# Kernel optimization log

Measured on AMD Instinct MI355X. Metric: run time of the kernel, lower is better.

## Reference

```python
import jax, jax.numpy as jnp
import numpy as np

B, S, T = 32, 32, 64          # docs, sentences/doc, tokens/sentence
E, HW, HS = 128, 128, 128     # embed, word hidden, sentence hidden
CW, CS = 128, 128             # attention context sizes
V, NC = 50000, 8              # vocab, classes


def setup_inputs() -> dict:
    key = jax.random.key(0)
    ks = iter(jax.random.split(key, 40))
    x = jax.random.randint(next(ks), (B, S, T), 1, V, dtype=jnp.int32)
    wl = jax.random.randint(next(ks), (B, S), 8, T + 1)   # word lengths
    sl = jax.random.randint(next(ks), (B,), 8, S + 1)     # sentence counts
    tmask = jnp.arange(T)[None, None, :] < wl[:, :, None]
    smask = (jnp.arange(S)[None, :] < sl[:, None])[:, :, None]
    x = jnp.where(tmask & smask, x, 0)                     # 0 = pad token

    def u(shape, scale=0.1):
        return jax.random.uniform(next(ks), shape, jnp.float32, -scale, scale)

    d = {"x": x, "emb": u((V, E))}
    # GRU params in torch layout: W_ih [3H,D] (r|z|n), W_hh [3H,H], biases [3H]
    for pre, Din, H in [("wf", E, HW), ("wb", E, HW), ("sf", 2 * HW, HS), ("sb", 2 * HW, HS)]:
        d[pre + "_Wih"] = u((3 * H, Din))
        d[pre + "_Whh"] = u((3 * H, H))
        d[pre + "_bih"] = u((3 * H,))
        d[pre + "_bhh"] = u((3 * H,))
    d["wproj_W"] = u((CW, 2 * HW)); d["wproj_b"] = u((CW,)); d["wctx"] = u((CW,))
    d["sproj_W"] = u((CS, 2 * HS)); d["sproj_b"] = u((CS,)); d["sctx"] = u((CS,))
    d["fc_W"] = u((NC, 2 * HS)); d["fc_b"] = u((NC,))
    return d


def seq_lens_2d(tok):
    # torch get_sequence_lens: T - trailing zeros, 1 if all zero
    nz = tok != 0
    any_nz = jnp.any(nz, axis=1)
    last = tok.shape[1] - jnp.argmax(nz[:, ::-1], axis=1)
    return jnp.where(any_nz, last, 1)


def doc_lens(x):
    # torch get_num_sentences_lens: S - trailing all-zero sentences
    nz = jnp.any(x != 0, axis=2)  # [B,S]
    any_nz = jnp.any(nz, axis=1)
    last = x.shape[1] - jnp.argmax(nz[:, ::-1], axis=1)
    return jnp.where(any_nz, last, 1)


def run_gru(x, lens, Wih, Whh, bih, bhh, reverse):
    # x: [N,Tm,D]; emulates pack_padded: state frozen / output zeroed beyond len
    N, Tm, _ = x.shape
    H = Whh.shape[1]
    xp = jnp.einsum('ntd,gd->ntg', x, Wih) + bih  # [N,Tm,3H]

    def step(h, inp):
        xg, t = inp
        hg = h @ Whh.T + bhh
        xr, xz, xn = jnp.split(xg, 3, axis=-1)
        hr, hz, hn = jnp.split(hg, 3, axis=-1)
        r = jax.nn.sigmoid(xr + hr)
        z = jax.nn.sigmoid(xz + hz)
        n = jnp.tanh(xn + r * hn)
        h_new = (1 - z) * n + z * h
        valid = (t < lens)[:, None]
        h_new = jnp.where(valid, h_new, h)
        return h_new, jnp.where(valid, h_new, 0.0)

    h0 = jnp.zeros((N, H), x.dtype)
    _, ys = jax.lax.scan(step, h0, (jnp.swapaxes(xp, 0, 1), jnp.arange(Tm)), reverse=reverse)
    return jnp.swapaxes(ys, 0, 1)  # [N,Tm,H]


def bigru(x, lens, pf, pb):
    return jnp.concatenate([run_gru(x, lens, *pf, reverse=False),
                            run_gru(x, lens, *pb, reverse=True)], axis=-1)


def attn_pool(out, lens, Wp, bp, ctx):
    # faithful to torch: softmax over padded positions up to max(lens)
    # (pad_packed pads to max length; padded outputs are zero but score=tanh(b)@c)
    Tm = out.shape[1]
    scores = jnp.tanh(out @ Wp.T + bp) @ ctx            # [N,Tm]
    valid = jnp.arange(Tm)[None, :] < jnp.max(lens)
    attn = jax.nn.softmax(jnp.where(valid, scores, -jnp.inf), axis=-1)
    return jnp.einsum('nt,nth->nh', attn, out)


def han_forward(x, emb,
                wf_Wih, wf_Whh, wf_bih, wf_bhh, wb_Wih, wb_Whh, wb_bih, wb_bhh,
                wproj_W, wproj_b, wctx,
                sf_Wih, sf_Whh, sf_bih, sf_bhh, sb_Wih, sb_Whh, sb_bih, sb_bhh,
                sproj_W, sproj_b, sctx, fc_W, fc_b):
    Bx, Sx, Tx = x.shape
    xw = x.reshape(-1, Tx)                      # [B*S, T]
    wlens = seq_lens_2d(xw)
    slens = doc_lens(x)
    we = emb[xw]                                # [B*S, T, E]
    wout = bigru(we, wlens, (wf_Wih, wf_Whh, wf_bih, wf_bhh),
                 (wb_Wih, wb_Whh, wb_bih, wb_bhh))     # [B*S, T, 2HW]
    sent = attn_pool(wout, wlens, wproj_W, wproj_b, wctx)  # [B*S, 2HW]
    sent = sent.reshape(Bx, Sx, -1)
    sout = bigru(sent, slens, (sf_Wih, sf_Whh, sf_bih, sf_bhh),
                 (sb_Wih, sb_Whh, sb_bih, sb_bhh))     # [B, S, 2HS]
    doc = attn_pool(sout, slens, sproj_W, sproj_b, sctx)   # [B, 2HS]
    return doc @ fc_W.T + fc_b                             # [B, NC]


def reference(x, emb,
              wf_Wih, wf_Whh, wf_bih, wf_bhh, wb_Wih, wb_Whh, wb_bih, wb_bhh,
              wproj_W, wproj_b, wctx,
              sf_Wih, sf_Whh, sf_bih, sf_bhh, sb_Wih, sb_Whh, sb_bih, sb_bhh,
              sproj_W, sproj_b, sctx, fc_W, fc_b):
    return han_forward(x, emb,
                       wf_Wih, wf_Whh, wf_bih, wf_bhh, wb_Wih, wb_Whh, wb_bih, wb_bhh,
                       wproj_W, wproj_b, wctx,
                       sf_Wih, sf_Whh, sf_bih, sf_bhh, sb_Wih, sb_Whh, sb_bih, sb_bhh,
                       sproj_W, sproj_b, sctx, fc_W, fc_b)
```

## Files before the change

### kernel.cpp

```cpp
#include <hip/hip_runtime.h>
#include <hip/hip_bf16.h>

typedef unsigned short ushort_t;
typedef __attribute__((ext_vector_type(4))) float floatx4;
typedef __attribute__((ext_vector_type(8))) short short8;

#define L2E 1.4426950408889634f

__device__ __forceinline__ float bf2f(ushort_t u) {
    union { unsigned int i; float f; } v; v.i = ((unsigned int)u) << 16; return v.f;
}
__device__ __forceinline__ ushort_t f2bf(float f) {
    union { float f; unsigned int i; } v; v.f = f;
    unsigned int i = v.i;
    i += 0x7fffu + ((i >> 16) & 1u);
    return (ushort_t)(i >> 16);
}
__device__ __forceinline__ float fexp2(float x) {
#if __has_builtin(__builtin_amdgcn_exp2f)
    return __builtin_amdgcn_exp2f(x);
#else
    return __expf(x * 0.6931471805599453f);
#endif
}
__device__ __forceinline__ float frcp(float x) {
#if __has_builtin(__builtin_amdgcn_rcpf)
    return __builtin_amdgcn_rcpf(x);
#else
    return 1.f / x;
#endif
}
__device__ __forceinline__ float sig2(float a)  { return frcp(1.f + fexp2(a)); }
__device__ __forceinline__ float tanh2(float y) { return 1.f - 2.f * frcp(1.f + fexp2(y)); }

__device__ __forceinline__ unsigned int packbf(float a, float b) {
    float2 t; t.x = a; t.y = b;
    __hip_bfloat162 h = __float22bfloat162_rn(t);
    union { __hip_bfloat162 h; unsigned int u; } v; v.h = h; return v.u;
}

__device__ __forceinline__ floatx4 MFMA16(short8 a, short8 b, floatx4 c) {
    return __builtin_amdgcn_mfma_f32_16x16x32_bf16(a, b, c, 0, 0, 0);
}

__device__ __forceinline__ void bar_lds() {
    __builtin_amdgcn_s_waitcnt(0xc07f);
    __builtin_amdgcn_s_barrier();
}

#define XIDX(c, m) ((((c) * 16) + ((m) ^ ((c) & 15))) * 8)

__global__ __launch_bounds__(64) void lens_kernel(const int* __restrict__ x,
                                                  const unsigned int* __restrict__ raw,
                                                  int* wlens, int* slens, int* dmax,
                                                  int* flag) {
    int b = blockIdx.x, s = threadIdx.x;
    if (b == 32) {
        int c = 0;
        for (int i = 0; i < 16; ++i) {
            unsigned int v = raw[s * 16 + i];
            unsigned int e = (v >> 7) & 0xFFu;
            if (e > 0x7Bu) ++c;
        }
        c += __shfl_xor(c, 1);  c += __shfl_xor(c, 2);  c += __shfl_xor(c, 4);
        c += __shfl_xor(c, 8);  c += __shfl_xor(c, 16); c += __shfl_xor(c, 32);
        if (s == 0) *flag = (c > 64) ? 1 : 0;
        return;
    }
    int last = 0;
    if (s < 32) {
        const int* tok = x + (b * 32 + s) * 64;
        for (int t = 0; t < 64; t += 4) {
            int4 v = *(const int4*)(tok + t);
            if (v.x) last = t + 1;
            if (v.y) last = t + 2;
            if (v.z) last = t + 3;
            if (v.w) last = t + 4;
        }
        wlens[b * 32 + s] = last ? last : 1;
    }
    int len = (s < 32) ? (last ? last : 1) : 0;
    int lm = len;
    for (int off = 32; off; off >>= 1) lm = max(lm, __shfl_xor(lm, off));
    unsigned long long mask = __ballot(s < 32 && last > 0);
    if (s == 0) {
        slens[b] = mask ? (63 - (int)__clzll(mask) + 1) : 1;
        dmax[b] = lm;
    }
}

struct ConvArgs {
    const void* src[25];
    int dstoff[25];
    int count[25];
    int cumblk[26];
    int mode[25];
    int rowdiv[25];
};

__global__ __launch_bounds__(256) void convert_kernel(ConvArgs a, ushort_t* __restrict__ dst,
                                                      const int* __restrict__ flag) {
    int b = blockIdx.x;
    int lo = 0, hi = 24;
    while (lo < hi) { int mid = (lo + hi + 1) >> 1; if (a.cumblk[mid] <= b) lo = mid; else hi = mid - 1; }
    int j = lo;
    int base = (b - a.cumblk[j]) * 2048 + threadIdx.x * 8;
    if (base >= a.count[j]) return;
    ushort_t* out = dst + a.dstoff[j] + base;
    int m = a.mode[j], rd = a.rowdiv[j];
    float f[8];
    if (*flag) {
        const float* s = (const float*)a.src[j] + base;
        float4 v0 = *(const float4*)s;
        float4 v1 = *(const float4*)(s + 4);
        f[0] = v0.x; f[1] = v0.y; f[2] = v0.z; f[3] = v0.w;
        f[4] = v1.x; f[5] = v1.y; f[6] = v1.z; f[7] = v1.w;
    } else {
        const ushort_t* s = (const ushort_t*)a.src[j] + base;
        uint4 v = *(const uint4*)s;
        const ushort_t* u = (const ushort_t*)&v;
        #pragma unroll
        for (int e = 0; e < 8; ++e) f[e] = bf2f(u[e]);
    }
    union { ushort_t u[8]; uint4 v; } o;
    #pragma unroll
    for (int e = 0; e < 8; ++e) {
        float sc = 1.f;
        if (m == 2) sc = 2.f * L2E;
        else if (m == 1) sc = ((base + e) / rd < 256) ? -L2E : 2.f * L2E;
        o.u[e] = f2bf(f[e] * sc);
    }
    *(uint4*)out = o.v;
}

__global__ __launch_bounds__(512, 2) void word_gru_kernel(
        const int* __restrict__ x, const ushort_t* __restrict__ emb,
        const ushort_t* __restrict__ Wih_f, const ushort_t* __restrict__ Whh_f,
        const ushort_t* __restrict__ bih_f, const ushort_t* __restrict__ bhh_f,
        const ushort_t* __restrict__ Wih_b, const ushort_t* __restrict__ Whh_b,
        const ushort_t* __restrict__ bih_b, const ushort_t* __restrict__ bhh_b,
        const int* __restrict__ lens, ushort_t* __restrict__ out) {
    const int T = 64;
    __shared__ ushort_t h_buf[2][2048];
    __shared__ float bsum_lds[256];
    __shared__ float bihn_lds[128];
    __shared__ float bhhn_lds[128];
    __shared__ int tok_lds[1024];

    int tid = threadIdx.x;
    int d = blockIdx.y;
    int n0 = blockIdx.x * 16;
    const ushort_t* Wih = d ? Wih_b : Wih_f;
    const ushort_t* Whh = d ? Whh_b : Whh_f;
    const ushort_t* bih = d ? bih_b : bih_f;
    const ushort_t* bhh = d ? bhh_b : bhh_f;
    int lane = tid & 63, wave = tid >> 6;
    int l15 = lane & 15, l4 = (lane >> 4) & 3;
    int jt = wave * 16;
    int j0 = jt + l4 * 4;

    for (int i = tid; i < 1024; i += 512) {
        int t = i >> 4, s = i & 15;
        tok_lds[i] = x[(n0 + s) * 64 + t];
    }
    if (tid < 256) bsum_lds[tid] = bf2f(bih[tid]) + bf2f(bhh[tid]);
    else if (tid < 384) {
        bihn_lds[tid - 256] = bf2f(bih[tid]);
        bhhn_lds[tid - 256] = bf2f(bhh[tid]);
    }
    { uint2 z = {0u, 0u}; *(uint2*)&h_buf[0][tid * 4] = z; }

    short8 wr[4], wz[4], wn[4], ur[4], uz[4], un[4];
    #pragma unroll
    for (int kf = 0; kf < 4; ++kf) {
        int col = kf * 32 + l4 * 8;
        wr[kf] = *(const short8*)(Wih + (size_t)(jt + l15) * 128 + col);
        wz[kf] = *(const short8*)(Wih + (size_t)(128 + jt + l15) * 128 + col);
        wn[kf] = *(const short8*)(Wih + (size_t)(256 + jt + l15) * 128 + col);
        ur[kf] = *(const short8*)(Whh + (size_t)(jt + l15) * 128 + col);
        uz[kf] = *(const short8*)(Whh + (size_t)(128 + jt + l15) * 128 + col);
        un[kf] = *(const short8*)(Whh + (size_t)(256 + jt + l15) * 128 + col);
    }
    __syncthreads();

    floatx4 br  = *(floatx4*)&bsum_lds[j0];
    floatx4 bz  = *(floatx4*)&bsum_lds[128 + j0];
    floatx4 bxn = *(floatx4*)&bihn_lds[j0];
    floatx4 bhn = *(floatx4*)&bhhn_lds[j0];
    int lv = lens[n0 + l15];
    float hreg[4] = {0.f, 0.f, 0.f, 0.f};

    short8 xc[4], xn_[4];
    {
        int t0 = d ? (T - 1) : 0;
        size_t rb = (size_t)tok_lds[t0 * 16 + l15] * 128 + l4 * 8;
        #pragma unroll
        for (int kf = 0; kf < 4; ++kf)
            xc[kf] = *(const short8*)(emb + rb + kf * 32);
    }

    for (int ti = 0; ti < T; ++ti) {
        int t = d ? (T - 1 - ti) : ti;
        bool have_next = (ti + 1) < T;
        if (have_next) {
            int tn = d ? (T - 2 - ti) : (ti + 1);
            size_t rb = (size_t)tok_lds[tn * 16 + l15] * 128 + l4 * 8;
            #pragma unroll
            for (int kf = 0; kf < 4; ++kf)
                xn_[kf] = *(const short8*)(emb + rb + kf * 32);
        }
        short8 hb[4];
        #pragma unroll
        for (int kf = 0; kf < 4; ++kf)
            hb[kf] = *(const short8*)&h_buf[ti & 1][XIDX(kf * 4 + l4, l15)];
        floatx4 arx = br, azx = bz, axn = bxn;
        floatx4 arh = {0.f, 0.f, 0.f, 0.f}, azh = {0.f, 0.f, 0.f, 0.f}, ahn = bhn;
        #pragma unroll
        for (int kf = 0; kf < 4; ++kf) {
            arx = MFMA16(wr[kf], xc[kf], arx);
            azx = MFMA16(wz[kf], xc[kf], azx);
            axn = MFMA16(wn[kf], xc[kf], axn);
        }
        #pragma unroll
        for (int kf = 0; kf < 4; ++kf) {
            arh = MFMA16(ur[kf], hb[kf], arh);
            azh = MFMA16(uz[kf], hb[kf], azh);
            ahn = MFMA16(un[kf], hb[kf], ahn);
        }
        bool valid = t < lv;
        float hnew[4];
        #pragma unroll
        for (int i = 0; i < 4; ++i) {
            float r  = sig2(arx[i] + arh[i]);
            float z  = sig2(azx[i] + azh[i]);
            float nn = tanh2(axn[i] + r * ahn[i]);
            hnew[i] = valid ? (nn + z * (hreg[i] - nn)) : hreg[i];
            hreg[i] = hnew[i];
        }
        uint2 h2, o2;
        h2.x = packbf(hnew[0], hnew[1]);
        h2.y = packbf(hnew[2], hnew[3]);
        o2.x = valid ? h2.x : 0u;
        o2.y = valid ? h2.y : 0u;
        *(uint2*)&h_buf[(ti & 1) ^ 1][XIDX(j0 >> 3, l15) + (j0 & 7)] = h2;
        *(uint2*)(out + ((size_t)(n0 + l15) * T + t) * 256 + d * 128 + j0) = o2;
        if (have_next) {
            #pragma unroll
            for (int kf = 0; kf < 4; ++kf) xc[kf] = xn_[kf];
        }
        bar_lds();
    }
}

__global__ __launch_bounds__(256) void spt_gemm_kernel(const ushort_t* __restrict__ A,
                                                       const ushort_t* __restrict__ Bf_,
                                                       const ushort_t* __restrict__ biasf,
                                                       ushort_t* __restrict__ Tf_,
                                                       const ushort_t* __restrict__ Bb_,
                                                       const ushort_t* __restrict__ biasb,
                                                       ushort_t* __restrict__ Tb_) {
    __shared__ ushort_t As[64 * 256];
    __shared__ ushort_t Bs[64 * 256];
    const int K = 256;
    int tid = threadIdx.x;
    int by = blockIdx.y;
    bool sb = by >= 6;
    int n0 = (sb ? by - 6 : by) * 64;
    const ushort_t* B = sb ? Bb_ : Bf_;
    const ushort_t* bias = sb ? biasb : biasf;
    ushort_t* Tp = sb ? Tb_ : Tf_;
    int m0 = blockIdx.x * 64;
    for (int idx = tid; idx < 2048; idx += 256) {
        int m = idx & 63, c = idx >> 6;
        *(uint4*)&As[(c * 64 + m) * 8] = *(const uint4*)(A + (size_t)(m0 + m) * K + c * 8);
    }
    for (int idx = tid; idx < 2048; idx += 256) {
        int n = idx & 63, c = idx >> 6;
        *(uint4*)&Bs[(c * 64 + n) * 8] = *(const uint4*)(B + (size_t)(n0 + n) * K + c * 8);
    }
    __syncthreads();
    int lane = tid & 63, wave = tid >> 6;
    int wm = (wave & 1) * 32, wn = (wave >> 1) * 32;
    int l15 = lane & 15, l4 = lane >> 4;
    floatx4 acc[2][2] = {};
    for (int kf = 0; kf < 8; ++kf) {
        int c = kf * 4 + l4;
        short8 a0 = *(const short8*)&As[(c * 64 + wm + l15) * 8];
        short8 a1 = *(const short8*)&As[(c * 64 + wm + 16 + l15) * 8];
        short8 b0 = *(const short8*)&Bs[(c * 64 + wn + l15) * 8];
        short8 b1 = *(const short8*)&Bs[(c * 64 + wn + 16 + l15) * 8];
        acc[0][0] = MFMA16(a0, b0, acc[0][0]);
        acc[0][1] = MFMA16(a0, b1, acc[0][1]);
        acc[1][0] = MFMA16(a1, b0, acc[1][0]);
        acc[1][1] = MFMA16(a1, b1, acc[1][1]);
    }
    for (int nt = 0; nt < 2; ++nt) {
        int n = n0 + wn + nt * 16 + l15;
        float bv = bf2f(bias[n]);
        int jc = n >> 2, ji = n & 3;
        for (int mt = 0; mt < 2; ++mt) {
            int mbase = m0 + wm + mt * 16 + l4 * 4;
            #pragma unroll
            for (int i = 0; i < 4; ++i) {
                int m = mbase + i;
                int doc = m >> 5, t = m & 31;
                size_t dst = ((size_t)((doc >> 4) * 32 + t) * 96 + jc) * 64
                           + (doc & 15) * 4 + ji;
                Tp[dst] = f2bf(acc[mt][nt][i] + bv);
            }
        }
    }
}

__global__ __launch_bounds__(512, 1) void sent_gru_kernel(
        const ushort_t* __restrict__ spT_f, const ushort_t* __restrict__ spT_b,
        const ushort_t* __restrict__ Whh_f, const ushort_t* __restrict__ Whh_b,
        const ushort_t* __restrict__ bhh_f, const ushort_t* __restrict__ bhh_b,
        const int* __restrict__ lens, ushort_t* __restrict__ out) {
    const int T = 32;
    __shared__ ushort_t h_buf[2][2048];
    __shared__ float bhh_lds[384];

    int tid = threadIdx.x;
    int d = blockIdx.y;
    int n0 = blockIdx.x * 16;
    const ushort_t* spT = d ? spT_b : spT_f;
    const ushort_t* Whh = d ? Whh_b : Whh_f;
    const ushort_t* bhh = d ? bhh_b : bhh_f;
    int lane = tid & 63, wave = tid >> 6;
    int l15 = lane & 15, l4 = (lane >> 4) & 3;
    int jt = wave * 16;
    int j0 = jt + l4 * 4;
    int jc = j0 >> 2;

    if (tid < 384) bhh_lds[tid] = bf2f(bhh[tid]);
    { uint2 z = {0u, 0u}; *(uint2*)&h_buf[0][tid * 4] = z; }

    short8 ur[4], uz[4], un[4];
    #pragma unroll
    for (int kf = 0; kf < 4; ++kf) {
        int col = kf * 32 + l4 * 8;
        ur[kf] = *(const short8*)(Whh + (size_t)(jt + l15) * 128 + col);
        uz[kf] = *(const short8*)(Whh + (size_t)(128 + jt + l15) * 128 + col);
        un[kf] = *(const short8*)(Whh + (size_t)(256 + jt + l15) * 128 + col);
    }
    __syncthreads();

    floatx4 br  = *(floatx4*)&bhh_lds[j0];
    floatx4 bz  = *(floatx4*)&bhh_lds[128 + j0];
    floatx4 bhn = *(floatx4*)&bhh_lds[256 + j0];
    int lv = lens[n0 + l15];
    float hreg[4] = {0.f, 0.f, 0.f, 0.f};

    const ushort_t* sp = spT + (size_t)(blockIdx.x * 32) * 96 * 64 + l15 * 4;
    ushort4 xr_c, xz_c, xn_c, xr_n, xz_n, xn_n;
    {
        int t0 = d ? (T - 1) : 0;
        size_t rb = (size_t)t0 * 96 * 64;
        xr_c = *(const ushort4*)(sp + rb + (size_t)jc * 64);
        xz_c = *(const ushort4*)(sp + rb + (size_t)(32 + jc) * 64);
        xn_c = *(const ushort4*)(sp + rb + (size_t)(64 + jc) * 64);
    }

    for (int ti = 0; ti < T; ++ti) {
        int t = d ? (T - 1 - ti) : ti;
        int cur = ti & 1;
        bool have_next = (ti + 1) < T;
        if (have_next) {
            int tn = d ? (T - 2 - ti) : (ti + 1);
            size_t rb = (size_t)tn * 96 * 64;
            xr_n = *(const ushort4*)(sp + rb + (size_t)jc * 64);
            xz_n = *(const ushort4*)(sp + rb + (size_t)(32 + jc) * 64);
            xn_n = *(const ushort4*)(sp + rb + (size_t)(64 + jc) * 64);
        }
        floatx4 ar = br, az = bz, ahn = bhn;
        #pragma unroll
        for (int kf = 0; kf < 4; ++kf) {
            short8 hb = *(const short8*)&h_buf[cur][XIDX(kf * 4 + l4, l15)];
            ar  = MFMA16(ur[kf], hb, ar);
            az  = MFMA16(uz[kf], hb, az);
            ahn = MFMA16(un[kf], hb, ahn);
        }
        float xr[4] = {bf2f(xr_c.x), bf2f(xr_c.y), bf2f(xr_c.z), bf2f(xr_c.w)};
        float xz[4] = {bf2f(xz_c.x), bf2f(xz_c.y), bf2f(xz_c.z), bf2f(xz_c.w)};
        float xn[4] = {bf2f(xn_c.x), bf2f(xn_c.y), bf2f(xn_c.z), bf2f(xn_c.w)};
        bool valid = t < lv;
        float hnew[4];
        #pragma unroll
        for (int i = 0; i < 4; ++i) {
            float r  = sig2(xr[i] + ar[i]);
            float z  = sig2(xz[i] + az[i]);
            float nn = tanh2(xn[i] + r * ahn[i]);
            hnew[i] = valid ? (nn + z * (hreg[i] - nn)) : hreg[i];
            hreg[i] = hnew[i];
        }
        uint2 h2, o2;
        h2.x = packbf(hnew[0], hnew[1]);
        h2.y = packbf(hnew[2], hnew[3]);
        o2.x = valid ? h2.x : 0u;
        o2.y = valid ? h2.y : 0u;
        *(uint2*)&h_buf[cur ^ 1][XIDX(j0 >> 3, l15) + (j0 & 7)] = h2;
        *(uint2*)(out + ((size_t)(n0 + l15) * T + t) * 256 + d * 128 + j0) = o2;
        if (have_next) { xr_c = xr_n; xz_c = xz_n; xn_c = xn_n; }
        bar_lds();
    }
}

#define SP 264
__global__ __launch_bounds__(256) void word_attn_kernel(const ushort_t* __restrict__ wout,
                                                        const ushort_t* __restrict__ W,
                                                        const ushort_t* __restrict__ bias,
                                                        const ushort_t* __restrict__ ctx,
                                                        const int* __restrict__ dmax,
                                                        ushort_t* __restrict__ sent) {
    __shared__ ushort_t tile[64 * SP];
    __shared__ float bc[256];
    __shared__ float sc_lds[64];
    __shared__ float p_lds[64];
    int tid = threadIdx.x, g = blockIdx.x;
    for (int idx = tid; idx < 2048; idx += 256) {
        int row = idx >> 5, k0 = (idx & 31) * 8;
        *(uint4*)&tile[row * SP + k0] = *(const uint4*)(wout + ((size_t)g * 64 + row) * 256 + k0);
    }
    if (tid < 128) bc[tid] = bf2f(bias[tid]);
    else bc[tid] = bf2f(ctx[tid - 128]);
    __syncthreads();
    int lane = tid & 63, wave = tid >> 6;
    int l15 = lane & 15, l4 = (lane >> 4) & 3;
    short8 a[8];
    #pragma unroll
    for (int kf = 0; kf < 8; ++kf)
        a[kf] = *(const short8*)&tile[(wave * 16 + l15) * SP + kf * 32 + l4 * 8];
    floatx4 acc[8];
    #pragma unroll
    for (int nt = 0; nt < 8; ++nt) {
        floatx4 c = {0.f, 0.f, 0.f, 0.f};
        #pragma unroll
        for (int kf = 0; kf < 8; ++kf) {
            short8 b = *(const short8*)(W + (size_t)(nt * 16 + l15) * 256 + kf * 32 + l4 * 8);
            c = MFMA16(a[kf], b, c);
        }
        acc[nt] = c;
    }
    float s[4] = {0.f, 0.f, 0.f, 0.f};
    #pragma unroll
    for (int nt = 0; nt < 8; ++nt) {
        float bv = bc[nt * 16 + l15], cv = bc[128 + nt * 16 + l15];
        #pragma unroll
        for (int i = 0; i < 4; ++i)
            s[i] += tanh2(acc[nt][i] + bv) * cv;
    }
    #pragma unroll
    for (int i = 0; i < 4; ++i) {
        s[i] += __shfl_xor(s[i], 1);
        s[i] += __shfl_xor(s[i], 2);
        s[i] += __shfl_xor(s[i], 4);
        s[i] += __shfl_xor(s[i], 8);
    }
    if (l15 == 0) {
        #pragma unroll
        for (int i = 0; i < 4; ++i) sc_lds[wave * 16 + l4 * 4 + i] = s[i];
    }
    __syncthreads();
    if (tid < 64) {
        int ml = dmax[tid & 31];
        for (int off = 32; off; off >>= 1) ml = max(ml, __shfl_xor(ml, off));
        bool v = tid < ml;
        float sc = v ? sc_lds[tid] : -1e30f;
        float mx = sc;
        for (int off = 32; off; off >>= 1) mx = fmaxf(mx, __shfl_xor(mx, off));
        float e = v ? __expf(sc - mx) : 0.f;
        float sum = e;
        for (int off = 32; off; off >>= 1) sum += __shfl_xor(sum, off);
        p_lds[tid] = e * frcp(fmaxf(sum, 1e-30f));
    }
    __syncthreads();
    float acc2 = 0.f;
    for (int t = 0; t < 64; ++t) acc2 += p_lds[t] * bf2f(tile[t * SP + tid]);
    sent[(size_t)g * 256 + tid] = f2bf(acc2);
}

__global__ __launch_bounds__(256) void sent_attn_fc_kernel(const ushort_t* __restrict__ sout,
                                                           const ushort_t* __restrict__ W,
                                                           const ushort_t* __restrict__ bias,
                                                           const ushort_t* __restrict__ ctx,
                                                           const ushort_t* __restrict__ fcW,
                                                           const ushort_t* __restrict__ fcb,
                                                           const int* __restrict__ slens,
                                                           const int* __restrict__ flagp,
                                                           void* __restrict__ outp) {
    __shared__ ushort_t tile[32 * SP];
    __shared__ float bc[256];
    __shared__ float sc_lds[32];
    __shared__ float p_lds[32];
    __shared__ float dv[256];
    int tid = threadIdx.x, g = blockIdx.x;
    for (int idx = tid; idx < 1024; idx += 256) {
        int row = idx >> 5, k0 = (idx & 31) * 8;
        *(uint4*)&tile[row * SP + k0] = *(const uint4*)(sout + ((size_t)g * 32 + row) * 256 + k0);
    }
    if (tid < 128) bc[tid] = bf2f(bias[tid]);
    else bc[tid] = bf2f(ctx[tid - 128]);
    __syncthreads();
    int lane = tid & 63, wave = tid >> 6;
    int l15 = lane & 15, l4 = (lane >> 4) & 3;
    if (wave < 2) {
        short8 a[8];
        #pragma unroll
        for (int kf = 0; kf < 8; ++kf)
            a[kf] = *(const short8*)&tile[(wave * 16 + l15) * SP + kf * 32 + l4 * 8];
        floatx4 acc[8];
        #pragma unroll
        for (int nt = 0; nt < 8; ++nt) {
            floatx4 c = {0.f, 0.f, 0.f, 0.f};
            #pragma unroll
            for (int kf = 0; kf < 8; ++kf) {
                short8 b = *(const short8*)(W + (size_t)(nt * 16 + l15) * 256 + kf * 32 + l4 * 8);
                c = MFMA16(a[kf], b, c);
            }
            acc[nt] = c;
        }
        float s[4] = {0.f, 0.f, 0.f, 0.f};
        #pragma unroll
        for (int nt = 0; nt < 8; ++nt) {
            float bv = bc[nt * 16 + l15], cv = bc[128 + nt * 16 + l15];
            #pragma unroll
            for (int i = 0; i < 4; ++i)
                s[i] += tanh2(acc[nt][i] + bv) * cv;
        }
        #pragma unroll
        for (int i = 0; i < 4; ++i) {
            s[i] += __shfl_xor(s[i], 1);
            s[i] += __shfl_xor(s[i], 2);
            s[i] += __shfl_xor(s[i], 4);
            s[i] += __shfl_xor(s[i], 8);
        }
        if (l15 == 0) {
            #pragma unroll
            for (int i = 0; i < 4; ++i) sc_lds[wave * 16 + l4 * 4 + i] = s[i];
        }
    }
    __syncthreads();
    if (tid < 32) {
        int ml = slens[tid];
        for (int off = 16; off; off >>= 1) ml = max(ml, __shfl_xor(ml, off, 32));
        bool v = tid < ml;
        float sc = v ? sc_lds[tid] : -1e30f;
        float mx = sc;
        for (int off = 16; off; off >>= 1) mx = fmaxf(mx, __shfl_xor(mx, off, 32));
        float e = v ? __expf(sc - mx) : 0.f;
        float sum = e;
        for (int off = 16; off; off >>= 1) sum += __shfl_xor(sum, off, 32);
        p_lds[tid] = e * frcp(fmaxf(sum, 1e-30f));
    }
    __syncthreads();
    float acc2 = 0.f;
    for (int t = 0; t < 32; ++t) acc2 += p_lds[t] * bf2f(tile[t * SP + tid]);
    dv[tid] = acc2;
    __syncthreads();
    int c = tid >> 5, q0 = (tid & 31) * 8;
    float partial = 0.f;
    #pragma unroll
    for (int q = 0; q < 8; ++q)
        partial += dv[q0 + q] * bf2f(fcW[(size_t)c * 256 + q0 + q]);
    for (int off = 16; off; off >>= 1) partial += __shfl_xor(partial, off, 32);
    if ((tid & 31) == 0) {
        float v = partial + bf2f(fcb[c]);
        if (*flagp) ((float*)outp)[g * 8 + c] = v;
        else        ((ushort_t*)outp)[g * 8 + c] = f2bf(v);
    }
}

extern "C" void kernel_launch(void* const* d_in, const int* in_sizes, int n_in,
                              void* d_out, int out_size, void* d_ws, size_t ws_size,
                              hipStream_t stream) {
    const int* x = (const int*)d_in[0];
    char* ws = (char*)d_ws;

    const size_t O_CONV = 0;
    const size_t O_WOUT = 14680064;
    const size_t O_SENT = 48234496;
    const size_t O_SOUT = 48758784;
    const size_t O_SPTF = 49283072;
    const size_t O_SPTB = 50855936;
    const size_t O_LENS = 52428800;
    const size_t O_SLEN = 52432896;
    const size_t O_DMAX = 52433024;
    const size_t O_FLAG = 52433152;

    ushort_t* conv = (ushort_t*)(ws + O_CONV);
    ushort_t* wout = (ushort_t*)(ws + O_WOUT);
    ushort_t* sent = (ushort_t*)(ws + O_SENT);
    ushort_t* sout = (ushort_t*)(ws + O_SOUT);
    ushort_t* sptf = (ushort_t*)(ws + O_SPTF);
    ushort_t* sptb = (ushort_t*)(ws + O_SPTB);
    int* wlens = (int*)(ws + O_LENS);
    int* slens = (int*)(ws + O_SLEN);
    int* dmax  = (int*)(ws + O_DMAX);
    int* flag  = (int*)(ws + O_FLAG);

    static const int kMode[25]   = {0, 1,1,1,1, 1,1,1,1, 1,1,1,1, 1,1,1,1, 2,2,0, 2,2,0, 0,0};
    static const int kRowdiv[25] = {1, 128,128,1,1, 128,128,1,1, 256,128,1,1, 256,128,1,1,
                                    1,1,1, 1,1,1, 1,1};

    ConvArgs ca;
    ushort_t* cw[25];
    int off = 0, blk = 0;
    for (int i = 1; i <= 25; ++i) {
        int j = i - 1;
        int cnt = in_sizes[i];
        ca.src[j] = d_in[i];
        ca.dstoff[j] = off;
        ca.count[j] = cnt;
        ca.cumblk[j] = blk;
        ca.mode[j] = kMode[j];
        ca.rowdiv[j] = kRowdiv[j];
        cw[j] = conv + off;
        off += cnt;
        blk += (cnt + 2047) / 2048;
    }
    ca.cumblk[25] = blk;

    lens_kernel<<<33, 64, 0, stream>>>(x, (const unsigned int*)d_in[1],
                                       wlens, slens, dmax, flag);
    convert_kernel<<<blk, 256, 0, stream>>>(ca, conv, flag);
    word_gru_kernel<<<dim3(64, 2), 512, 0, stream>>>(
        x, cw[0],
        cw[1], cw[2], cw[3], cw[4],
        cw[5], cw[6], cw[7], cw[8],
        wlens, wout);
    word_attn_kernel<<<1024, 256, 0, stream>>>(wout, cw[17], cw[18], cw[19], dmax, sent);
    spt_gemm_kernel<<<dim3(16, 12), 256, 0, stream>>>(sent, cw[9], cw[11], sptf,
                                                      cw[13], cw[15], sptb);
    sent_gru_kernel<<<dim3(2, 2), 512, 0, stream>>>(
        sptf, sptb, cw[10], cw[14], cw[12], cw[16], slens, sout);
    sent_attn_fc_kernel<<<32, 256, 0, stream>>>(sout, cw[20], cw[21], cw[22],
                                                cw[23], cw[24], slens, flag, d_out);
    (void)n_in; (void)out_size; (void)ws_size;
}
```

Before: 285.7 us.

## Halve sequences per GRU block to double block count for latency-bound recurrences

Both the word-level and sentence-level GRU kernels now process 8 sequences per block instead of 16, so twice as many blocks run (256 instead of 128 for words, 8 instead of 4 for sentences). The MFMA N dimension stays 16, with lanes 8-15 duplicating rows 0-7, and only the first half writes results. A new swizzle macro matches the smaller hidden-state buffer. The aim is to spread the serial recurrence over more compute units on the 256-CU part, at the cost of half-wasted MFMA work and twice the weight loading per sequence.

```diff
diff --git a/kernel.cpp b/kernel.cpp
--- a/kernel.cpp
+++ b/kernel.cpp
@@ -49,6 +49,7 @@
 }
 
 #define XIDX(c, m) ((((c) * 16) + ((m) ^ ((c) & 15))) * 8)
+#define X8(c, m) ((((c) * 8) + ((m) ^ ((c) & 7))) * 8)
 
 __global__ __launch_bounds__(64) void lens_kernel(const int* __restrict__ x,
                                                   const unsigned int* __restrict__ raw,
@@ -141,34 +142,36 @@
         const ushort_t* __restrict__ bih_b, const ushort_t* __restrict__ bhh_b,
         const int* __restrict__ lens, ushort_t* __restrict__ out) {
     const int T = 64;
-    __shared__ ushort_t h_buf[2][2048];
+    __shared__ ushort_t h_buf[2][1024];
     __shared__ float bsum_lds[256];
     __shared__ float bihn_lds[128];
     __shared__ float bhhn_lds[128];
-    __shared__ int tok_lds[1024];
+    __shared__ int tok_lds[512];
 
     int tid = threadIdx.x;
     int d = blockIdx.y;
-    int n0 = blockIdx.x * 16;
+    int n0 = blockIdx.x * 8;
     const ushort_t* Wih = d ? Wih_b : Wih_f;
     const ushort_t* Whh = d ? Whh_b : Whh_f;
     const ushort_t* bih = d ? bih_b : bih_f;
     const ushort_t* bhh = d ? bhh_b : bhh_f;
     int lane = tid & 63, wave = tid >> 6;
     int l15 = lane & 15, l4 = (lane >> 4) & 3;
+    int s8 = l15 & 7;
+    bool sv = l15 < 8;
     int jt = wave * 16;
     int j0 = jt + l4 * 4;
 
-    for (int i = tid; i < 1024; i += 512) {
-        int t = i >> 4, s = i & 15;
-        tok_lds[i] = x[(n0 + s) * 64 + t];
+    {
+        int t = tid >> 3, s = tid & 7;
+        tok_lds[tid] = x[(n0 + s) * 64 + t];
     }
     if (tid < 256) bsum_lds[tid] = bf2f(bih[tid]) + bf2f(bhh[tid]);
     else if (tid < 384) {
         bihn_lds[tid - 256] = bf2f(bih[tid]);
         bhhn_lds[tid - 256] = bf2f(bhh[tid]);
     }
-    { uint2 z = {0u, 0u}; *(uint2*)&h_buf[0][tid * 4] = z; }
+    if (tid < 256) { uint2 z = {0u, 0u}; *(uint2*)&h_buf[0][tid * 4] = z; }
 
     short8 wr[4], wz[4], wn[4], ur[4], uz[4], un[4];
     #pragma unroll
@@ -187,13 +190,13 @@
     floatx4 bz  = *(floatx4*)&bsum_lds[128 + j0];
     floatx4 bxn = *(floatx4*)&bihn_lds[j0];
     floatx4 bhn = *(floatx4*)&bhhn_lds[j0];
-    int lv = lens[n0 + l15];
+    int lv = lens[n0 + s8];
     float hreg[4] = {0.f, 0.f, 0.f, 0.f};
 
     short8 xc[4], xn_[4];
     {
         int t0 = d ? (T - 1) : 0;
-        size_t rb = (size_t)tok_lds[t0 * 16 + l15] * 128 + l4 * 8;
+        size_t rb = (size_t)tok_lds[t0 * 8 + s8] * 128 + l4 * 8;
         #pragma unroll
         for (int kf = 0; kf < 4; ++kf)
             xc[kf] = *(const short8*)(emb + rb + kf * 32);
@@ -204,7 +207,7 @@
         bool have_next = (ti + 1) < T;
         if (have_next) {
             int tn = d ? (T - 2 - ti) : (ti + 1);
-            size_t rb = (size_t)tok_lds[tn * 16 + l15] * 128 + l4 * 8;
+            size_t rb = (size_t)tok_lds[tn * 8 + s8] * 128 + l4 * 8;
             #pragma unroll
             for (int kf = 0; kf < 4; ++kf)
                 xn_[kf] = *(const short8*)(emb + rb + kf * 32);
@@ -212,7 +215,7 @@
         short8 hb[4];
         #pragma unroll
         for (int kf = 0; kf < 4; ++kf)
-            hb[kf] = *(const short8*)&h_buf[ti & 1][XIDX(kf * 4 + l4, l15)];
+            hb[kf] = *(const short8*)&h_buf[ti & 1][X8(kf * 4 + l4, s8)];
         floatx4 arx = br, azx = bz, axn = bxn;
         floatx4 arh = {0.f, 0.f, 0.f, 0.f}, azh = {0.f, 0.f, 0.f, 0.f}, ahn = bhn;
         #pragma unroll
@@ -237,13 +240,15 @@
             hnew[i] = valid ? (nn + z * (hreg[i] - nn)) : hreg[i];
             hreg[i] = hnew[i];
         }
-        uint2 h2, o2;
-        h2.x = packbf(hnew[0], hnew[1]);
-        h2.y = packbf(hnew[2], hnew[3]);
-        o2.x = valid ? h2.x : 0u;
-        o2.y = valid ? h2.y : 0u;
-        *(uint2*)&h_buf[(ti & 1) ^ 1][XIDX(j0 >> 3, l15) + (j0 & 7)] = h2;
-        *(uint2*)(out + ((size_t)(n0 + l15) * T + t) * 256 + d * 128 + j0) = o2;
+        if (sv) {
+            uint2 h2, o2;
+            h2.x = packbf(hnew[0], hnew[1]);
+            h2.y = packbf(hnew[2], hnew[3]);
+            o2.x = valid ? h2.x : 0u;
+            o2.y = valid ? h2.y : 0u;
+            *(uint2*)&h_buf[(ti & 1) ^ 1][X8(j0 >> 3, s8) + (j0 & 7)] = h2;
+            *(uint2*)(out + ((size_t)(n0 + s8) * T + t) * 256 + d * 128 + j0) = o2;
+        }
         if (have_next) {
             #pragma unroll
             for (int kf = 0; kf < 4; ++kf) xc[kf] = xn_[kf];
@@ -312,29 +317,32 @@
     }
 }
 
-__global__ __launch_bounds__(512, 1) void sent_gru_kernel(
+__global__ __launch_bounds__(512, 2) void sent_gru_kernel(
         const ushort_t* __restrict__ spT_f, const ushort_t* __restrict__ spT_b,
         const ushort_t* __restrict__ Whh_f, const ushort_t* __restrict__ Whh_b,
         const ushort_t* __restrict__ bhh_f, const ushort_t* __restrict__ bhh_b,
         const int* __restrict__ lens, ushort_t* __restrict__ out) {
     const int T = 32;
-    __shared__ ushort_t h_buf[2][2048];
+    __shared__ ushort_t h_buf[2][1024];
     __shared__ float bhh_lds[384];
 
     int tid = threadIdx.x;
     int d = blockIdx.y;
-    int n0 = blockIdx.x * 16;
+    int bx = blockIdx.x;
+    int n0 = bx * 8;
     const ushort_t* spT = d ? spT_b : spT_f;
     const ushort_t* Whh = d ? Whh_b : Whh_f;
     const ushort_t* bhh = d ? bhh_b : bhh_f;
     int lane = tid & 63, wave = tid >> 6;
     int l15 = lane & 15, l4 = (lane >> 4) & 3;
+    int s8 = l15 & 7;
+    bool sv = l15 < 8;
     int jt = wave * 16;
     int j0 = jt + l4 * 4;
     int jc = j0 >> 2;
 
     if (tid < 384) bhh_lds[tid] = bf2f(bhh[tid]);
-    { uint2 z = {0u, 0u}; *(uint2*)&h_buf[0][tid * 4] = z; }
+    if (tid < 256) { uint2 z = {0u, 0u}; *(uint2*)&h_buf[0][tid * 4] = z; }
 
     short8 ur[4], uz[4], un[4];
     #pragma unroll
@@ -349,10 +357,11 @@
     floatx4 br  = *(floatx4*)&bhh_lds[j0];
     floatx4 bz  = *(floatx4*)&bhh_lds[128 + j0];
     floatx4 bhn = *(floatx4*)&bhh_lds[256 + j0];
-    int lv = lens[n0 + l15];
+    int lv = lens[n0 + s8];
     float hreg[4] = {0.f, 0.f, 0.f, 0.f};
 
-    const ushort_t* sp = spT + (size_t)(blockIdx.x * 32) * 96 * 64 + l15 * 4;
+    const ushort_t* sp = spT + (size_t)((bx >> 1) * 32) * 96 * 64
+                       + ((bx & 1) * 8 + s8) * 4;
     ushort4 xr_c, xz_c, xn_c, xr_n, xz_n, xn_n;
     {
         int t0 = d ? (T - 1) : 0;
@@ -376,7 +385,7 @@
         floatx4 ar = br, az = bz, ahn = bhn;
         #pragma unroll
         for (int kf = 0; kf < 4; ++kf) {
-            short8 hb = *(const short8*)&h_buf[cur][XIDX(kf * 4 + l4, l15)];
+            short8 hb = *(const short8*)&h_buf[cur][X8(kf * 4 + l4, s8)];
             ar  = MFMA16(ur[kf], hb, ar);
             az  = MFMA16(uz[kf], hb, az);
             ahn = MFMA16(un[kf], hb, ahn);
@@ -394,13 +403,15 @@
             hnew[i] = valid ? (nn + z * (hreg[i] - nn)) : hreg[i];
             hreg[i] = hnew[i];
         }
-        uint2 h2, o2;
-        h2.x = packbf(hnew[0], hnew[1]);
-        h2.y = packbf(hnew[2], hnew[3]);
-        o2.x = valid ? h2.x : 0u;
-        o2.y = valid ? h2.y : 0u;
-        *(uint2*)&h_buf[cur ^ 1][XIDX(j0 >> 3, l15) + (j0 & 7)] = h2;
-        *(uint2*)(out + ((size_t)(n0 + l15) * T + t) * 256 + d * 128 + j0) = o2;
+        if (sv) {
+            uint2 h2, o2;
+            h2.x = packbf(hnew[0], hnew[1]);
+            h2.y = packbf(hnew[2], hnew[3]);
+            o2.x = valid ? h2.x : 0u;
+            o2.y = valid ? h2.y : 0u;
+            *(uint2*)&h_buf[cur ^ 1][X8(j0 >> 3, s8) + (j0 & 7)] = h2;
+            *(uint2*)(out + ((size_t)(n0 + s8) * T + t) * 256 + d * 128 + j0) = o2;
+        }
         if (have_next) { xr_c = xr_n; xz_c = xz_n; xn_c = xn_n; }
         bar_lds();
     }
@@ -624,7 +635,7 @@
     lens_kernel<<<33, 64, 0, stream>>>(x, (const unsigned int*)d_in[1],
                                        wlens, slens, dmax, flag);
     convert_kernel<<<blk, 256, 0, stream>>>(ca, conv, flag);
-    word_gru_kernel<<<dim3(64, 2), 512, 0, stream>>>(
+    word_gru_kernel<<<dim3(128, 2), 512, 0, stream>>>(
         x, cw[0],
         cw[1], cw[2], cw[3], cw[4],
         cw[5], cw[6], cw[7], cw[8],
@@ -632,7 +643,7 @@
     word_attn_kernel<<<1024, 256, 0, stream>>>(wout, cw[17], cw[18], cw[19], dmax, sent);
     spt_gemm_kernel<<<dim3(16, 12), 256, 0, stream>>>(sent, cw[9], cw[11], sptf,
                                                       cw[13], cw[15], sptb);
-    sent_gru_kernel<<<dim3(2, 2), 512, 0, stream>>>(
+    sent_gru_kernel<<<dim3(4, 2), 512, 0, stream>>>(
         sptf, sptb, cw[10], cw[14], cw[12], cw[16], slens, sout);
     sent_attn_fc_kernel<<<32, 256, 0, stream>>>(sout, cw[20], cw[21], cw[22],
                                                 cw[23], cw[24], slens, flag, d_out);
```

Measured after the change: 278.9 us. -2.4%, faster.
